# Kernel optimization log

Hardware: AMD Instinct MI355X
Metric: run time of the kernel (lower is better)

## Reference

```python
import jax, jax.numpy as jnp
import numpy as np

NUM_HEADS = 8
LN_EPS = 1e-5


def layer_norm(x, g, b):
    mu = jnp.mean(x, axis=-1, keepdims=True)
    var = jnp.var(x, axis=-1, keepdims=True)
    return (x - mu) * jax.lax.rsqrt(var + LN_EPS) * g + b


def mha(q, k, v, in_w, in_b, out_w, out_b):
    # torch nn.MultiheadAttention (batch_first): packed in_proj (3D,D), out_proj (D,D)
    B, Lq, D = q.shape
    Lk = k.shape[1]
    H = NUM_HEADS
    dh = D // H
    wq, wk, wv = in_w[:D], in_w[D:2 * D], in_w[2 * D:]
    bq, bk, bv = in_b[:D], in_b[D:2 * D], in_b[2 * D:]
    qp = (q @ wq.T + bq).reshape(B, Lq, H, dh).transpose(0, 2, 1, 3)
    kp = (k @ wk.T + bk).reshape(B, Lk, H, dh).transpose(0, 2, 1, 3)
    vp = (v @ wv.T + bv).reshape(B, Lk, H, dh).transpose(0, 2, 1, 3)
    scores = jnp.einsum('bhqd,bhkd->bhqk', qp, kp) / jnp.sqrt(jnp.asarray(dh, q.dtype))
    attn = jax.nn.softmax(scores, axis=-1)  # (B,H,Lq,Lk)
    out = jnp.einsum('bhqk,bhkd->bhqd', attn, vp)
    out = out.transpose(0, 2, 1, 3).reshape(B, Lq, D)
    return out @ out_w.T + out_b, attn


def setup_inputs() -> dict:
    key = jax.random.key(0)
    ks = jax.random.split(key, 8)
    B, P, Q, D = 32, 576, 256, 768
    s = 0.02
    return {
        'image_tokens': jax.random.normal(ks[0], (B, 1 + P, D), jnp.float32),
        'tactile_tokens': jax.random.normal(ks[1], (B, Q, D), jnp.float32),
        't2i_in_w': jax.random.normal(ks[2], (3 * D, D), jnp.float32) * s,
        't2i_in_b': jnp.zeros((3 * D,), jnp.float32),
        't2i_out_w': jax.random.normal(ks[3], (D, D), jnp.float32) * s,
        't2i_out_b': jnp.zeros((D,), jnp.float32),
        'i2t_in_w': jax.random.normal(ks[4], (3 * D, D), jnp.float32) * s,
        'i2t_in_b': jnp.zeros((3 * D,), jnp.float32),
        'i2t_out_w': jax.random.normal(ks[5], (D, D), jnp.float32) * s,
        'i2t_out_b': jnp.zeros((D,), jnp.float32),
        'ln_tact_g': jnp.ones((D,), jnp.float32),
        'ln_tact_b': jnp.zeros((D,), jnp.float32),
        'ln_img_g': jnp.ones((D,), jnp.float32),
        'ln_img_b': jnp.zeros((D,), jnp.float32),
    }


def reference(image_tokens, tactile_tokens, t2i_in_w, t2i_in_b, t2i_out_w, t2i_out_b,
              i2t_in_w, i2t_in_b, i2t_out_w, i2t_out_b,
              ln_tact_g, ln_tact_b, ln_img_g, ln_img_b):
    # attention_type == 'all_patch'
    cls_tok = image_tokens[:, :1, :]
    patch_tok = image_tokens[:, 1:, :]
    tact_out, attn_weights = mha(tactile_tokens, patch_tok, patch_tok,
                                 t2i_in_w, t2i_in_b, t2i_out_w, t2i_out_b)
    tactile_tokens = layer_norm(tactile_tokens + tact_out, ln_tact_g, ln_tact_b)
    patch_out, _ = mha(patch_tok, tactile_tokens, tactile_tokens,
                       i2t_in_w, i2t_in_b, i2t_out_w, i2t_out_b)
    patch_tok = layer_norm(patch_tok + patch_out, ln_img_g, ln_img_b)
    image_tokens = jnp.concatenate([cls_tok, patch_tok], axis=1)
    return image_tokens, tactile_tokens, attn_weights
```

## Files before the change

kernel.cpp:

```cpp
#include <hip/hip_runtime.h>
#include <stdint.h>
#include <math.h>

typedef unsigned short u16;
typedef __attribute__((ext_vector_type(8))) short bf16x8;
typedef __attribute__((ext_vector_type(4))) float f32x4;

__device__ __forceinline__ u16 f2b(float f) {
    unsigned u = __float_as_uint(f);
    u = (u + 0x7FFFu + ((u >> 16) & 1u)) >> 16;
    return (u16)u;
}

__device__ __forceinline__ void gload16(const void* g, void* lds) {
    __builtin_amdgcn_global_load_lds(
        (const __attribute__((address_space(1))) unsigned int*)(uintptr_t)g,
        (__attribute__((address_space(3))) unsigned int*)(unsigned int)(uintptr_t)lds,
        16, 0, 0);
}

#define BM 128
#define BN 128
#define BK 32

struct GemmGrp {
    const u16* A; const u16* B; const float* bias; const float* resid;
    float* Cf; u16* Cb;
    int M, N, lda, ldb, ldc;
    float scale;
    int rgrp; long long rgA, rgoff; int ldr;
};
struct G3 { GemmGrp g[3]; int start[4]; int K; };

__global__ __launch_bounds__(256) void gemm_grp(G3 P)
{
    __shared__ __align__(16) u16 lA[2][BM * BK];
    __shared__ __align__(16) u16 lB[2][BN * BK];

    const int tid = threadIdx.x;
    const int wave = tid >> 6;
    const int lane = tid & 63;

    const int ntot = P.start[3];
    int L = blockIdx.x;
    if ((ntot & 7) == 0) L = (L & 7) * (ntot >> 3) + (L >> 3);

    const int gi = (L >= P.start[1]) + (L >= P.start[2]);
    GemmGrp g;
    if (gi == 0) g = P.g[0]; else if (gi == 1) g = P.g[1]; else g = P.g[2];
    const int t = L - P.start[gi];

    const int tilesN = g.N / BN;
    const int tm = t / tilesN;
    const int tn = t % tilesN;
    const int row0 = tm * BM;
    const int col0 = tn * BN;

    const int f0 = tid * 8;
    const int f1 = (256 + tid) * 8;
    const int sr0 = f0 >> 5, sc0 = f0 & 31;
    const int sr1 = f1 >> 5, sc1 = f1 & 31;

    const u16* pa0 = g.A + (long long)(row0 + sr0) * g.lda + sc0;
    const u16* pa1 = g.A + (long long)(row0 + sr1) * g.lda + sc1;
    const u16* pb0 = g.B + (long long)(col0 + sr0) * g.ldb + sc0;
    const u16* pb1 = g.B + (long long)(col0 + sr1) * g.ldb + sc1;

    const int wr = wave >> 1, wc = wave & 1;
    const int fr = lane & 15;
    const int kk = (lane >> 4) * 8;

    f32x4 acc[4][4];
    #pragma unroll
    for (int m = 0; m < 4; ++m)
        #pragma unroll
        for (int n = 0; n < 4; ++n) {
            f32x4 z = {0.f, 0.f, 0.f, 0.f};
            acc[m][n] = z;
        }

    #define STAGE(buf, k0) do { \
        gload16(pa0 + (k0), &lA[buf][(wave * 64) * 8]); \
        gload16(pa1 + (k0), &lA[buf][2048 + (wave * 64) * 8]); \
        gload16(pb0 + (k0), &lB[buf][(wave * 64) * 8]); \
        gload16(pb1 + (k0), &lB[buf][2048 + (wave * 64) * 8]); \
    } while (0)

    STAGE(0, 0);
    __syncthreads();
    int cur = 0;
    for (int k0 = 0; k0 < P.K; k0 += BK) {
        if (k0 + BK < P.K) STAGE(cur ^ 1, k0 + BK);
        bf16x8 af[4], bfv[4];
        #pragma unroll
        for (int m = 0; m < 4; ++m)
            af[m] = *(const bf16x8*)&lA[cur][(wr * 64 + m * 16 + fr) * BK + kk];
        #pragma unroll
        for (int n = 0; n < 4; ++n)
            bfv[n] = *(const bf16x8*)&lB[cur][(wc * 64 + n * 16 + fr) * BK + kk];
        #pragma unroll
        for (int m = 0; m < 4; ++m)
            #pragma unroll
            for (int n = 0; n < 4; ++n)
                acc[m][n] = __builtin_amdgcn_mfma_f32_16x16x32_bf16(af[m], bfv[n], acc[m][n], 0, 0, 0);
        __syncthreads();
        cur ^= 1;
    }
    #undef STAGE

    const int orow = row0 + wr * 64;
    const int ocol = col0 + wc * 64;
    const int g4 = (lane >> 4) * 4;
    float bcol[4];
    #pragma unroll
    for (int n = 0; n < 4; ++n)
        bcol[n] = g.bias ? g.bias[ocol + n * 16 + fr] : 0.f;

    #pragma unroll
    for (int m = 0; m < 4; ++m) {
        #pragma unroll
        for (int j = 0; j < 4; ++j) {
            const int r = orow + m * 16 + g4 + j;
            long long ro = 0;
            if (g.resid) {
                unsigned q = (unsigned)r / (unsigned)g.rgrp;
                unsigned rem = (unsigned)r - q * (unsigned)g.rgrp;
                ro = (long long)q * g.rgA + (long long)rem * g.ldr + g.rgoff;
            }
            const long long crow = (long long)r * g.ldc;
            #pragma unroll
            for (int n = 0; n < 4; ++n) {
                const int c = ocol + n * 16 + fr;
                float v = acc[m][n][j] * g.scale + bcol[n];
                if (g.resid) v += g.resid[ro + c];
                if (g.Cb) g.Cb[crow + c] = f2b(v);
                else      g.Cf[crow + c] = v;
            }
        }
    }
}

template <bool WATTN>
__global__ __launch_bounds__(256, 2) void fused_attn(
    const u16* __restrict__ Q, const u16* __restrict__ K, const u16* __restrict__ Vt,
    float* __restrict__ attn, u16* __restrict__ O,
    int Lq, int Lk, int ldq, int ldk, int ldo)
{
    __shared__ __align__(16) u16 lQP[128 * 96];
    __shared__ __align__(16) u16 lKt[64 * 96];
    __shared__ __align__(16) u16 lVt[96 * 64];
    __shared__ float lM2[2][128], lL2[2][128];

    const int tid = threadIdx.x, wave = tid >> 6, lane = tid & 63;
    const int fr = lane & 15, g = lane >> 4;
    const int wr = wave >> 1, wc = wave & 1;
    const int z = blockIdx.y, b = z >> 3, h = z & 7;
    const int q0 = blockIdx.x * 128;
    const int nt = Lk >> 6;

    const u16* Qz = Q + (long long)b * Lq * ldq + h * 96;
    const u16* Kz = K + (long long)b * Lk * ldk + h * 96;
    const u16* Vz = Vt + (long long)z * 96 * Lk;
    u16* Oz = O + (long long)b * Lq * ldo + h * 96;
    float* Az = attn + (long long)z * Lq * Lk;

    const u16* qsrc[6];
    #pragma unroll
    for (int t = 0; t < 6; ++t) {
        int u = t * 256 + tid;
        int r = u / 12, cu = u % 12;
        int qr = q0 + r; if (qr > Lq - 1) qr = Lq - 1;
        qsrc[t] = Qz + (long long)qr * ldq + cu * 8;
    }
    const u16* ksrc[3];
    #pragma unroll
    for (int t = 0; t < 3; ++t) {
        int u = t * 256 + tid;
        int r = u / 12, cu = u % 12;
        ksrc[t] = Kz + (long long)r * ldk + cu * 8;
    }
    const u16* vsrc[3];
    #pragma unroll
    for (int t = 0; t < 3; ++t) {
        int u = t * 256 + tid;
        int d = u >> 3, uu = u & 7;
        vsrc[t] = Vz + (long long)d * Lk + ((uu ^ (d & 7)) * 8);
    }
    const long long kstep = 64LL * ldk;

    #define DQ(t) ((char*)lQP + ((t) * 256 + wave * 64) * 16)
    #define DK(t) ((char*)lKt + ((t) * 256 + wave * 64) * 16)
    #define DV(t) ((char*)lVt + ((t) * 256 + wave * 64) * 16)

    #pragma unroll
    for (int t = 0; t < 6; ++t) gload16(qsrc[t], DQ(t));
    #pragma unroll
    for (int t = 0; t < 3; ++t) gload16(ksrc[t], DK(t));
    __syncthreads();

    bf16x8 qf[4][3];
    #pragma unroll
    for (int m = 0; m < 4; ++m)
        #pragma unroll
        for (int ks = 0; ks < 3; ++ks)
            qf[m][ks] = *(const bf16x8*)((const char*)lQP + (wr * 64 + m * 16 + fr) * 192 + ks * 64 + g * 16);

    float m_run[4], l_run[4];
    #pragma unroll
    for (int i = 0; i < 4; ++i) { m_run[i] = -1e30f; l_run[i] = 0.f; }

    for (int i = 0; i < nt; ++i) {
        bf16x8 kf[2][3];
        #pragma unroll
        for (int mk = 0; mk < 2; ++mk)
            #pragma unroll
            for (int ks = 0; ks < 3; ++ks)
                kf[mk][ks] = *(const bf16x8*)((const char*)lKt + (wc * 32 + mk * 16 + fr) * 192 + ks * 64 + g * 16);
        f32x4 sa[2][4];
        #pragma unroll
        for (int mk = 0; mk < 2; ++mk)
            #pragma unroll
            for (int nq = 0; nq < 4; ++nq) {
                f32x4 zz = {0.f, 0.f, 0.f, 0.f};
                sa[mk][nq] = zz;
            }
        #pragma unroll
        for (int ks = 0; ks < 3; ++ks)
            #pragma unroll
            for (int mk = 0; mk < 2; ++mk)
                #pragma unroll
                for (int nq = 0; nq < 4; ++nq)
                    sa[mk][nq] = __builtin_amdgcn_mfma_f32_16x16x32_bf16(kf[mk][ks], qf[nq][ks], sa[mk][nq], 0, 0, 0);
        #pragma unroll
        for (int nq = 0; nq < 4; ++nq) {
            float tmx = -1e30f;
            #pragma unroll
            for (int mk = 0; mk < 2; ++mk)
                #pragma unroll
                for (int j = 0; j < 4; ++j)
                    tmx = fmaxf(tmx, sa[mk][nq][j]);
            tmx = fmaxf(tmx, __shfl_xor(tmx, 16));
            tmx = fmaxf(tmx, __shfl_xor(tmx, 32));
            const float mnew = fmaxf(m_run[nq], tmx);
            float ts = 0.f;
            #pragma unroll
            for (int mk = 0; mk < 2; ++mk)
                #pragma unroll
                for (int j = 0; j < 4; ++j)
                    ts += __expf(sa[mk][nq][j] - mnew);
            ts += __shfl_xor(ts, 16);
            ts += __shfl_xor(ts, 32);
            l_run[nq] = l_run[nq] * __expf(m_run[nq] - mnew) + ts;
            m_run[nq] = mnew;
        }
        __syncthreads();
        if (i + 1 < nt) {
            #pragma unroll
            for (int t = 0; t < 3; ++t) { ksrc[t] += kstep; gload16(ksrc[t], DK(t)); }
        }
        __syncthreads();
    }

    if (g == 0) {
        #pragma unroll
        for (int nq = 0; nq < 4; ++nq) {
            lM2[wc][wr * 64 + nq * 16 + fr] = m_run[nq];
            lL2[wc][wr * 64 + nq * 16 + fr] = l_run[nq];
        }
    }
    #pragma unroll
    for (int t = 0; t < 3; ++t) ksrc[t] -= (long long)(nt - 1) * kstep;
    #pragma unroll
    for (int t = 0; t < 3; ++t) gload16(ksrc[t], DK(t));
    #pragma unroll
    for (int t = 0; t < 3; ++t) gload16(vsrc[t], DV(t));
    __syncthreads();

    float mrow[16], linv[16];
    #pragma unroll
    for (int m = 0; m < 4; ++m)
        #pragma unroll
        for (int j = 0; j < 4; ++j) {
            const int q = wr * 64 + m * 16 + g * 4 + j;
            const float ma = lM2[0][q], mb = lM2[1][q];
            const float mm = fmaxf(ma, mb);
            const float ll = lL2[0][q] * __expf(ma - mm) + lL2[1][q] * __expf(mb - mm);
            mrow[m * 4 + j] = mm;
            linv[m * 4 + j] = 1.f / ll;
        }

    f32x4 oacc[4][3];
    #pragma unroll
    for (int m = 0; m < 4; ++m)
        #pragma unroll
        for (int nd = 0; nd < 3; ++nd) {
            f32x4 zz = {0.f, 0.f, 0.f, 0.f};
            oacc[m][nd] = zz;
        }

    for (int i = 0; i < nt; ++i) {
        const int k0 = i * 64;
        bf16x8 kf[2][3];
        #pragma unroll
        for (int n = 0; n < 2; ++n)
            #pragma unroll
            for (int ks = 0; ks < 3; ++ks)
                kf[n][ks] = *(const bf16x8*)((const char*)lKt + (wc * 32 + n * 16 + fr) * 192 + ks * 64 + g * 16);
        f32x4 ss[4][2];
        #pragma unroll
        for (int m = 0; m < 4; ++m)
            #pragma unroll
            for (int n = 0; n < 2; ++n) {
                f32x4 zz = {0.f, 0.f, 0.f, 0.f};
                ss[m][n] = zz;
            }
        #pragma unroll
        for (int ks = 0; ks < 3; ++ks)
            #pragma unroll
            for (int m = 0; m < 4; ++m)
                #pragma unroll
                for (int n = 0; n < 2; ++n)
                    ss[m][n] = __builtin_amdgcn_mfma_f32_16x16x32_bf16(qf[m][ks], kf[n][ks], ss[m][n], 0, 0, 0);
        __syncthreads();
        if (i + 1 < nt) {
            #pragma unroll
            for (int t = 0; t < 3; ++t) { ksrc[t] += kstep; gload16(ksrc[t], DK(t)); }
        }
        #pragma unroll
        for (int m = 0; m < 4; ++m)
            #pragma unroll
            for (int n = 0; n < 2; ++n)
                #pragma unroll
                for (int j = 0; j < 4; ++j) {
                    const float p = __expf(ss[m][n][j] - mrow[m * 4 + j]) * linv[m * 4 + j];
                    const int q = wr * 64 + m * 16 + g * 4 + j;
                    const int k = wc * 32 + n * 16 + fr;
                    if (WATTN) Az[(long long)(q0 + q) * Lk + k0 + k] = p;
                    *(u16*)((char*)lQP + q * 144 + k * 2) = f2b(p);
                }
        __syncthreads();
        #pragma unroll
        for (int ks = 0; ks < 2; ++ks) {
            bf16x8 vf[3], pf[4];
            #pragma unroll
            for (int nd = 0; nd < 3; ++nd) {
                const int row = wc * 48 + nd * 16 + fr;
                vf[nd] = *(const bf16x8*)((const char*)lVt + row * 128 + (((ks * 4 + g) ^ (row & 7)) * 16));
            }
            #pragma unroll
            for (int m = 0; m < 4; ++m)
                pf[m] = *(const bf16x8*)((const char*)lQP + (wr * 64 + m * 16 + fr) * 144 + ks * 64 + g * 16);
            #pragma unroll
            for (int m = 0; m < 4; ++m)
                #pragma unroll
                for (int nd = 0; nd < 3; ++nd)
                    oacc[m][nd] = __builtin_amdgcn_mfma_f32_16x16x32_bf16(pf[m], vf[nd], oacc[m][nd], 0, 0, 0);
        }
        __syncthreads();
        if (i + 1 < nt) {
            #pragma unroll
            for (int t = 0; t < 3; ++t) { vsrc[t] += 64; gload16(vsrc[t], DV(t)); }
        }
    }

    #pragma unroll
    for (int m = 0; m < 4; ++m)
        #pragma unroll
        for (int j = 0; j < 4; ++j) {
            const int q = q0 + wr * 64 + m * 16 + g * 4 + j;
            if (q < Lq) {
                #pragma unroll
                for (int nd = 0; nd < 3; ++nd) {
                    const int c = wc * 48 + nd * 16 + fr;
                    Oz[(long long)q * ldo + c] = f2b(oacc[m][nd][j]);
                }
            }
        }
    #undef DQ
    #undef DK
    #undef DV
}

__global__ __launch_bounds__(256) void transpose_v(
    const u16* __restrict__ V, u16* __restrict__ Vt, int L, int ldv)
{
    __shared__ unsigned int t[64 * 97];
    const int z = blockIdx.y;
    const int b = z >> 3, h = z & 7;
    const int l0 = blockIdx.x * 64;
    const int tid = threadIdx.x;
    for (int i = 0; i < 24; ++i) {
        const int idx = tid + i * 256;
        const int l = idx / 96, d = idx % 96;
        t[l * 97 + d] = V[((long long)(b * L + l0 + l)) * ldv + h * 96 + d];
    }
    __syncthreads();
    for (int i = 0; i < 24; ++i) {
        const int idx = tid + i * 256;
        const int d = idx / 64, l = idx % 64;
        Vt[((long long)z * 96 + d) * L + l0 + l] = (u16)t[l * 97 + d];
    }
}

__global__ __launch_bounds__(256) void ln_k(
    const float* __restrict__ X, const float* __restrict__ g, const float* __restrict__ b,
    float* __restrict__ outF, u16* __restrict__ outB,
    int rows, int grp, long long gA, long long goff, int ldo)
{
    const int wave = threadIdx.x >> 6, lane = threadIdx.x & 63;
    const int row = blockIdx.x * 4 + wave;
    if (row >= rows) return;
    const float* x = X + (long long)row * 768;
    float v[12], s = 0.f, sq = 0.f;
    #pragma unroll
    for (int i = 0; i < 12; ++i) { v[i] = x[lane + 64 * i]; s += v[i]; sq += v[i] * v[i]; }
    #pragma unroll
    for (int o = 32; o; o >>= 1) { s += __shfl_xor(s, o); sq += __shfl_xor(sq, o); }
    const float mu = s * (1.f / 768.f);
    const float var = sq * (1.f / 768.f) - mu * mu;
    const float inv = rsqrtf(var + 1e-5f);
    const long long ob = (long long)(row / grp) * gA + (long long)(row % grp) * ldo + goff;
    #pragma unroll
    for (int i = 0; i < 12; ++i) {
        const int c = lane + 64 * i;
        const float y = (v[i] - mu) * inv * g[c] + b[c];
        outF[ob + c] = y;
        if (outB) outB[(long long)row * 768 + c] = f2b(y);
    }
}

__global__ __launch_bounds__(256) void conv_f2b(
    const float4* __restrict__ in, u16* __restrict__ out, long long n4)
{
    long long i = (long long)blockIdx.x * 256 + threadIdx.x;
    const long long stride = (long long)gridDim.x * 256;
    for (; i < n4; i += stride) {
        const float4 f = in[i];
        ushort4 u;
        u.x = f2b(f.x); u.y = f2b(f.y); u.z = f2b(f.z); u.w = f2b(f.w);
        ((ushort4*)out)[i] = u;
    }
}

__global__ __launch_bounds__(256) void conv_w4(
    const float4* __restrict__ a, const float4* __restrict__ b,
    const float4* __restrict__ c, const float4* __restrict__ d,
    u16* __restrict__ oa, u16* __restrict__ ob,
    u16* __restrict__ oc, u16* __restrict__ od)
{
    const long long n1 = 442368, n2 = 589824, n3 = 1032192, n4 = 1179648;
    long long i = (long long)blockIdx.x * 256 + threadIdx.x;
    const long long stride = (long long)gridDim.x * 256;
    for (; i < n4; i += stride) {
        const float4* src; u16* dst; long long k;
        if (i < n1)      { src = a; dst = oa; k = i; }
        else if (i < n2) { src = b; dst = ob; k = i - n1; }
        else if (i < n3) { src = c; dst = oc; k = i - n2; }
        else             { src = d; dst = od; k = i - n3; }
        const float4 f = src[k];
        ushort4 u;
        u.x = f2b(f.x); u.y = f2b(f.y); u.z = f2b(f.z); u.w = f2b(f.w);
        ((ushort4*)dst)[k] = u;
    }
}

__global__ __launch_bounds__(256) void conv_patch(
    const float* __restrict__ img, u16* __restrict__ out)
{
    long long i = (long long)blockIdx.x * 256 + threadIdx.x;
    const long long n4 = 18432LL * 192;
    const long long stride = (long long)gridDim.x * 256;
    for (; i < n4; i += stride) {
        const long long r = i / 192; const int c4 = (int)(i % 192);
        const long long sr = (r / 576) * 577 + 1 + (r % 576);
        const float4 f = ((const float4*)img)[sr * 192 + c4];
        ushort4 u;
        u.x = f2b(f.x); u.y = f2b(f.y); u.z = f2b(f.z); u.w = f2b(f.w);
        ((ushort4*)out)[i] = u;
    }
}

__global__ __launch_bounds__(256) void cls_copy(
    const float* __restrict__ img, float* __restrict__ out)
{
    const int i = blockIdx.x * 256 + threadIdx.x;
    if (i < 32 * 768) {
        const int b = i / 768, c = i % 768;
        out[(long long)b * 577 * 768 + c] = img[(long long)b * 577 * 768 + c];
    }
}

static inline GemmGrp mkgrp(const u16* A, const u16* B, const float* bias,
    const float* resid, float* Cf, u16* Cb, int M, int N, int lda, int ldb,
    int ldc, float scale, int rgrp, long long rgA, long long rgoff, int ldr)
{
    GemmGrp g;
    g.A = A; g.B = B; g.bias = bias; g.resid = resid; g.Cf = Cf; g.Cb = Cb;
    g.M = M; g.N = N; g.lda = lda; g.ldb = ldb; g.ldc = ldc;
    g.scale = scale; g.rgrp = rgrp; g.rgA = rgA; g.rgoff = rgoff; g.ldr = ldr;
    return g;
}

static inline void launch_grp(hipStream_t s, const GemmGrp* gs, int ng, int K)
{
    G3 P;
    P.start[0] = 0;
    for (int i = 0; i < 3; ++i) {
        const GemmGrp& src = gs[i < ng ? i : ng - 1];
        P.g[i] = src;
        const int nb = (i < ng) ? (src.M / BM) * (src.N / BN) : 0;
        P.start[i + 1] = P.start[i] + nb;
    }
    P.K = K;
    gemm_grp<<<dim3((unsigned)P.start[3]), dim3(256), 0, s>>>(P);
}

extern "C" void kernel_launch(void* const* d_in, const int* in_sizes, int n_in,
                              void* d_out, int out_size, void* d_ws, size_t ws_size,
                              hipStream_t stream)
{
    (void)in_sizes; (void)n_in; (void)out_size; (void)ws_size;
    const float* img   = (const float*)d_in[0];
    const float* tac   = (const float*)d_in[1];
    const float* w1in  = (const float*)d_in[2];
    const float* b1in  = (const float*)d_in[3];
    const float* w1out = (const float*)d_in[4];
    const float* b1out = (const float*)d_in[5];
    const float* w2in  = (const float*)d_in[6];
    const float* b2in  = (const float*)d_in[7];
    const float* w2out = (const float*)d_in[8];
    const float* b2out = (const float*)d_in[9];
    const float* lng1  = (const float*)d_in[10];
    const float* lnb1  = (const float*)d_in[11];
    const float* lng2  = (const float*)d_in[12];
    const float* lnb2  = (const float*)d_in[13];
    float* out = (float*)d_out;

    const long long o_tac  = 32LL * 577 * 768;
    const long long o_attn = o_tac + 32LL * 256 * 768;
    const float qscale = 1.0f / sqrtf(96.0f);

    u16* p = (u16*)d_ws;
    u16* tact_bf    = p; p += 8192LL * 768;
    u16* patch_bf   = p; p += 18432LL * 768;
    u16* w1in_bf    = p; p += 2304LL * 768;
    u16* w1out_bf   = p; p += 768LL * 768;
    u16* w2in_bf    = p; p += 2304LL * 768;
    u16* w2out_bf   = p; p += 768LL * 768;
    u16* tactnew_bf = p; p += 8192LL * 768;
    u16* Q1  = p; p += 8192LL * 768;
    u16* KV1 = p; p += 18432LL * 1536;
    u16* Vt1 = p; p += 256LL * 96 * 576;
    u16* AO1 = p; p += 8192LL * 768;
    u16* Q2  = p; p += 18432LL * 768;
    u16* KV2 = p; p += 8192LL * 1536;
    u16* Vt2 = p; p += 256LL * 96 * 256;
    u16* AO2 = p; p += 18432LL * 768;
    float* O1s = (float*)p; p += 2LL * 8192 * 768;
    float* O2s = (float*)p; p += 2LL * 18432 * 768;

    conv_f2b<<<1024, 256, 0, stream>>>((const float4*)tac, tact_bf, 8192LL * 192);
    conv_patch<<<1024, 256, 0, stream>>>(img, patch_bf);
    conv_w4<<<1024, 256, 0, stream>>>(
        (const float4*)w1in, (const float4*)w1out, (const float4*)w2in, (const float4*)w2out,
        w1in_bf, w1out_bf, w2in_bf, w2out_bf);
    cls_copy<<<96, 256, 0, stream>>>(img, out);

    {
        GemmGrp gs[3] = {
            mkgrp(tact_bf,  w1in_bf,              b1in,       nullptr, nullptr, Q1,
                  8192, 768, 768, 768, 768, qscale, 1, 0, 0, 0),
            mkgrp(patch_bf, w1in_bf + 768LL*768,  b1in + 768, nullptr, nullptr, KV1,
                  18432, 1536, 768, 768, 1536, 1.0f, 1, 0, 0, 0),
            mkgrp(patch_bf, w2in_bf,              b2in,       nullptr, nullptr, Q2,
                  18432, 768, 768, 768, 768, qscale, 1, 0, 0, 0)
        };
        launch_grp(stream, gs, 3, 768);
    }

    transpose_v<<<dim3(9, 256), 256, 0, stream>>>(KV1 + 768, Vt1, 576, 1536);
    fused_attn<true><<<dim3(2, 256), 256, 0, stream>>>(
        Q1, KV1, Vt1, out + o_attn, AO1, 256, 576, 768, 1536, 768);
    {
        GemmGrp g = mkgrp(AO1, w1out_bf, b1out, tac, O1s, nullptr,
                          8192, 768, 768, 768, 768, 1.0f, 1, 768, 0, 0);
        launch_grp(stream, &g, 1, 768);
    }
    ln_k<<<8192 / 4, 256, 0, stream>>>(O1s, lng1, lnb1, out + o_tac, tactnew_bf,
        8192, 8192, 0, 0, 768);

    {
        GemmGrp g = mkgrp(tactnew_bf, w2in_bf + 768LL*768, b2in + 768, nullptr,
                          nullptr, KV2, 8192, 1536, 768, 768, 1536, 1.0f, 1, 0, 0, 0);
        launch_grp(stream, &g, 1, 768);
    }
    transpose_v<<<dim3(4, 256), 256, 0, stream>>>(KV2 + 768, Vt2, 256, 1536);
    fused_attn<false><<<dim3(5, 256), 256, 0, stream>>>(
        Q2, KV2, Vt2, nullptr, AO2, 576, 256, 768, 1536, 768);
    {
        GemmGrp g = mkgrp(AO2, w2out_bf, b2out, img, O2s, nullptr,
                          18432, 768, 768, 768, 768, 1.0f, 576, 577LL * 768, 768, 768);
        launch_grp(stream, &g, 1, 768);
    }
    ln_k<<<18432 / 4, 256, 0, stream>>>(O2s, lng2, lnb2, out, nullptr,
        18432, 576, 577LL * 768, 768, 768);
}
```

Measured before the change: 764.8 us.

## Double-buffer K/V tiles in fused attention and raise priority around MFMA

```diff
diff --git a/kernel.cpp b/kernel.cpp
--- a/kernel.cpp
+++ b/kernel.cpp
@@ -147,8 +147,8 @@
     int Lq, int Lk, int ldq, int ldk, int ldo)
 {
     __shared__ __align__(16) u16 lQP[128 * 96];
-    __shared__ __align__(16) u16 lKt[64 * 96];
-    __shared__ __align__(16) u16 lVt[96 * 64];
+    __shared__ __align__(16) u16 lKt[2][64 * 96];
+    __shared__ __align__(16) u16 lVt[2][96 * 64];
     __shared__ float lM2[2][128], lL2[2][128];
 
     const int tid = threadIdx.x, wave = tid >> 6, lane = tid & 63;
@@ -188,14 +188,14 @@
     }
     const long long kstep = 64LL * ldk;
 
-    #define DQ(t) ((char*)lQP + ((t) * 256 + wave * 64) * 16)
-    #define DK(t) ((char*)lKt + ((t) * 256 + wave * 64) * 16)
-    #define DV(t) ((char*)lVt + ((t) * 256 + wave * 64) * 16)
+    #define DQ(t)    ((char*)lQP + ((t) * 256 + wave * 64) * 16)
+    #define DK(bf,t) ((char*)lKt[bf] + ((t) * 256 + wave * 64) * 16)
+    #define DV(bf,t) ((char*)lVt[bf] + ((t) * 256 + wave * 64) * 16)
 
     #pragma unroll
     for (int t = 0; t < 6; ++t) gload16(qsrc[t], DQ(t));
     #pragma unroll
-    for (int t = 0; t < 3; ++t) gload16(ksrc[t], DK(t));
+    for (int t = 0; t < 3; ++t) gload16(ksrc[t], DK(0, t));
     __syncthreads();
 
     bf16x8 qf[4][3];
@@ -209,13 +209,18 @@
     #pragma unroll
     for (int i = 0; i < 4; ++i) { m_run[i] = -1e30f; l_run[i] = 0.f; }
 
+    int buf = 0;
     for (int i = 0; i < nt; ++i) {
+        if (i + 1 < nt) {
+            #pragma unroll
+            for (int t = 0; t < 3; ++t) { ksrc[t] += kstep; gload16(ksrc[t], DK(buf ^ 1, t)); }
+        }
         bf16x8 kf[2][3];
         #pragma unroll
         for (int mk = 0; mk < 2; ++mk)
             #pragma unroll
             for (int ks = 0; ks < 3; ++ks)
-                kf[mk][ks] = *(const bf16x8*)((const char*)lKt + (wc * 32 + mk * 16 + fr) * 192 + ks * 64 + g * 16);
+                kf[mk][ks] = *(const bf16x8*)((const char*)lKt[buf] + (wc * 32 + mk * 16 + fr) * 192 + ks * 64 + g * 16);
         f32x4 sa[2][4];
         #pragma unroll
         for (int mk = 0; mk < 2; ++mk)
@@ -224,6 +229,7 @@
                 f32x4 zz = {0.f, 0.f, 0.f, 0.f};
                 sa[mk][nq] = zz;
             }
+        __builtin_amdgcn_s_setprio(1);
         #pragma unroll
         for (int ks = 0; ks < 3; ++ks)
             #pragma unroll
@@ -231,6 +237,7 @@
                 #pragma unroll
                 for (int nq = 0; nq < 4; ++nq)
                     sa[mk][nq] = __builtin_amdgcn_mfma_f32_16x16x32_bf16(kf[mk][ks], qf[nq][ks], sa[mk][nq], 0, 0, 0);
+        __builtin_amdgcn_s_setprio(0);
         #pragma unroll
         for (int nq = 0; nq < 4; ++nq) {
             float tmx = -1e30f;
@@ -254,11 +261,7 @@
             m_run[nq] = mnew;
         }
         __syncthreads();
-        if (i + 1 < nt) {
-            #pragma unroll
-            for (int t = 0; t < 3; ++t) { ksrc[t] += kstep; gload16(ksrc[t], DK(t)); }
-        }
-        __syncthreads();
+        buf ^= 1;
     }
 
     if (g == 0) {
@@ -271,9 +274,9 @@
     #pragma unroll
     for (int t = 0; t < 3; ++t) ksrc[t] -= (long long)(nt - 1) * kstep;
     #pragma unroll
-    for (int t = 0; t < 3; ++t) gload16(ksrc[t], DK(t));
-    #pragma unroll
-    for (int t = 0; t < 3; ++t) gload16(vsrc[t], DV(t));
+    for (int t = 0; t < 3; ++t) gload16(ksrc[t], DK(0, t));
+    #pragma unroll
+    for (int t = 0; t < 3; ++t) gload16(vsrc[t], DV(0, t));
     __syncthreads();
 
     float mrow[16], linv[16];
@@ -298,14 +301,21 @@
             oacc[m][nd] = zz;
         }
 
+    buf = 0;
     for (int i = 0; i < nt; ++i) {
         const int k0 = i * 64;
+        if (i + 1 < nt) {
+            #pragma unroll
+            for (int t = 0; t < 3; ++t) { ksrc[t] += kstep; gload16(ksrc[t], DK(buf ^ 1, t)); }
+            #pragma unroll
+            for (int t = 0; t < 3; ++t) { vsrc[t] += 64;    gload16(vsrc[t], DV(buf ^ 1, t)); }
+        }
         bf16x8 kf[2][3];
         #pragma unroll
         for (int n = 0; n < 2; ++n)
             #pragma unroll
             for (int ks = 0; ks < 3; ++ks)
-                kf[n][ks] = *(const bf16x8*)((const char*)lKt + (wc * 32 + n * 16 + fr) * 192 + ks * 64 + g * 16);
+                kf[n][ks] = *(const bf16x8*)((const char*)lKt[buf] + (wc * 32 + n * 16 + fr) * 192 + ks * 64 + g * 16);
         f32x4 ss[4][2];
         #pragma unroll
         for (int m = 0; m < 4; ++m)
@@ -314,6 +324,7 @@
                 f32x4 zz = {0.f, 0.f, 0.f, 0.f};
                 ss[m][n] = zz;
             }
+        __builtin_amdgcn_s_setprio(1);
         #pragma unroll
         for (int ks = 0; ks < 3; ++ks)
             #pragma unroll
@@ -321,11 +332,7 @@
                 #pragma unroll
                 for (int n = 0; n < 2; ++n)
                     ss[m][n] = __builtin_amdgcn_mfma_f32_16x16x32_bf16(qf[m][ks], kf[n][ks], ss[m][n], 0, 0, 0);
-        __syncthreads();
-        if (i + 1 < nt) {
-            #pragma unroll
-            for (int t = 0; t < 3; ++t) { ksrc[t] += kstep; gload16(ksrc[t], DK(t)); }
-        }
+        __builtin_amdgcn_s_setprio(0);
         #pragma unroll
         for (int m = 0; m < 4; ++m)
             #pragma unroll
@@ -339,13 +346,14 @@
                     *(u16*)((char*)lQP + q * 144 + k * 2) = f2b(p);
                 }
         __syncthreads();
+        __builtin_amdgcn_s_setprio(1);
         #pragma unroll
         for (int ks = 0; ks < 2; ++ks) {
             bf16x8 vf[3], pf[4];
             #pragma unroll
             for (int nd = 0; nd < 3; ++nd) {
                 const int row = wc * 48 + nd * 16 + fr;
-                vf[nd] = *(const bf16x8*)((const char*)lVt + row * 128 + (((ks * 4 + g) ^ (row & 7)) * 16));
+                vf[nd] = *(const bf16x8*)((const char*)lVt[buf] + row * 128 + (((ks * 4 + g) ^ (row & 7)) * 16));
             }
             #pragma unroll
             for (int m = 0; m < 4; ++m)
@@ -356,11 +364,9 @@
                 for (int nd = 0; nd < 3; ++nd)
                     oacc[m][nd] = __builtin_amdgcn_mfma_f32_16x16x32_bf16(pf[m], vf[nd], oacc[m][nd], 0, 0, 0);
         }
+        __builtin_amdgcn_s_setprio(0);
         __syncthreads();
-        if (i + 1 < nt) {
-            #pragma unroll
-            for (int t = 0; t < 3; ++t) { vsrc[t] += 64; gload16(vsrc[t], DV(t)); }
-        }
+        buf ^= 1;
     }
 
     #pragma unroll
```

Result: no change. 763.8 us (-0.1%).
